# Optimization experiments

Hardware: AMD Instinct MI355X
Metric: run time of the kernel (lower is better)

The kernel has to match this reference:

```python
import jax, jax.numpy as jnp
import numpy as np

N, V, C_IN, C_OUT = 8, 2048, 32, 64
ORDER, SUPPORT_LEN = 2, 3
BN_EPS = 1e-5


def _make_adj(key):
    a = jax.random.uniform(key, (N, V, V), dtype=jnp.float32)
    # row-normalize like a diffusion transition matrix
    return a / jnp.sum(a, axis=-1, keepdims=True)


def setup_inputs() -> dict:
    key = jax.random.key(0)
    ks = jax.random.split(key, 6)
    x = jax.random.normal(ks[0], (N, V, C_IN), dtype=jnp.float32)
    A0 = _make_adj(ks[1])
    A1 = _make_adj(ks[2])
    A2 = _make_adj(ks[3])
    c_in_total = (ORDER * SUPPORT_LEN + 1) * C_IN  # 224
    W = jax.random.normal(ks[4], (C_OUT, c_in_total), dtype=jnp.float32) / np.sqrt(c_in_total)
    b = jnp.zeros((C_OUT,), dtype=jnp.float32)
    gamma = jnp.ones((C_OUT,), dtype=jnp.float32)
    beta = jnp.zeros((C_OUT,), dtype=jnp.float32)
    return {"x": x, "A0": A0, "A1": A1, "A2": A2, "W": W, "b": b,
            "gamma": gamma, "beta": beta}


def reference(x, A0, A1, A2, W, b, gamma, beta):
    # nconv: einsum('nvl,nvw->nwl')
    nconv = lambda h, a: jnp.einsum('nvl,nvw->nwl', h, a)
    out = [x]
    for a in (A0, A1, A2):
        x1 = nconv(x, a)
        out.append(x1)
        for _ in range(2, ORDER + 1):
            x2 = nconv(x1, a)
            out.append(x2)
            x1 = x2
    h = jnp.concatenate(out, axis=-1)            # [N, V, 7*C_IN]
    # 1x1 Conv1d over channel axis == pointwise matmul + bias
    h = jnp.einsum('nvc,oc->nvo', h, W) + b      # [N, V, C_OUT]
    # BatchNorm1d (training-mode batch stats over batch and node dims)
    mean = jnp.mean(h, axis=(0, 1))
    var = jnp.var(h, axis=(0, 1))
    h = (h - mean) * jax.lax.rsqrt(var + BN_EPS) * gamma + beta
    # dropout p=0.0 -> identity
    return h
```

## Files before the change

kernel.cpp:

```cpp
#include <hip/hip_runtime.h>
#include <hip/hip_bf16.h>


#define V    2048
#define NB   8
#define CIN  32
#define COUT 64
#define CTOT 224

typedef __attribute__((ext_vector_type(8))) short bf16x8;
typedef __attribute__((ext_vector_type(16))) float f32x16;

static __device__ __forceinline__ short f2bf(float f) {
  __hip_bfloat16 h = __float2bfloat16(f);
  return *reinterpret_cast<short*>(&h);
}

static __device__ __forceinline__ void gll16(const float* g, float* l) {
  __builtin_amdgcn_global_load_lds(
      (const __attribute__((address_space(1))) void*)g,
      (__attribute__((address_space(3))) void*)l, 16, 0, 0);
}

__global__ __launch_bounds__(256) void nconv_mfma_kernel(
    const float* __restrict__ Adj, const float* __restrict__ Xin,
    float* __restrict__ Xout) {
  __shared__ float S[4][4][2][16][32];

  const int bid  = blockIdx.x;
  const int n    = bid >> 6;
  const int ws   = (bid & 63) * 32;
  const int t    = threadIdx.x;
  const int q    = t >> 6;
  const int lane = t & 63;
  const int g    = lane >> 5;
  const int mn   = lane & 31;

  const float* Abase = Adj + (size_t)n * V * V + (size_t)q * 512 * V + ws;
  const float* Xbase = Xin + (size_t)n * V * CIN + q * 512 * CIN;
  const float* Asrc = Abase + (size_t)(lane >> 3) * V + (lane & 7) * 4;
  const float* Xsrc = Xbase + lane * 4;

  auto stage = [&](int c) {
    const int r = c & 3;
    const float* a = Asrc + (size_t)c * 16 * V;
    const float* x = Xsrc + c * 16 * CIN;
    gll16(a,         &S[q][r][0][0][0]);
    gll16(a + 8 * V, &S[q][r][0][8][0]);
    gll16(x,         &S[q][r][1][0][0]);
    gll16(x + 256,   &S[q][r][1][8][0]);
  };

  f32x16 acc;
#pragma unroll
  for (int r = 0; r < 16; ++r) acc[r] = 0.f;

  auto compute = [&](int r) {
    float a8[8], x8[8];
#pragma unroll
    for (int j = 0; j < 8; ++j) {
      a8[j] = S[q][r][0][8 * g + j][mn];
      x8[j] = S[q][r][1][8 * g + j][mn];
    }
    bf16x8 aop, bop;
#pragma unroll
    for (int j = 0; j < 8; ++j) {
      aop[j] = f2bf(x8[j]);
      bop[j] = f2bf(a8[j]);
    }
    acc = __builtin_amdgcn_mfma_f32_32x32x16_bf16(aop, bop, acc, 0, 0, 0);
  };

  stage(0);
  stage(1);
  stage(2);
#pragma unroll 1
  for (int kk = 0; kk < 29; ++kk) {
    stage(kk + 3);
    asm volatile("s_waitcnt vmcnt(12)" ::: "memory");
    __builtin_amdgcn_sched_barrier(0);
    compute(kk & 3);
  }
  asm volatile("s_waitcnt vmcnt(8)" ::: "memory");
  __builtin_amdgcn_sched_barrier(0);
  compute(29 & 3);
  asm volatile("s_waitcnt vmcnt(4)" ::: "memory");
  __builtin_amdgcn_sched_barrier(0);
  compute(30 & 3);
  asm volatile("s_waitcnt vmcnt(0)" ::: "memory");
  __builtin_amdgcn_sched_barrier(0);
  compute(31 & 3);

  __syncthreads();
  float(*Lred)[32][33] = reinterpret_cast<float(*)[32][33]>(&S[0][0][0][0][0]);
#pragma unroll
  for (int r = 0; r < 16; ++r) {
    Lred[q][(r & 3) + 8 * (r >> 2) + 4 * g][mn] = acc[r];
  }
  __syncthreads();
  const int w  = t >> 3;
  const int l4 = t & 7;
  float4 o;
  float* op = &o.x;
#pragma unroll
  for (int i = 0; i < 4; ++i) {
    op[i] = Lred[0][l4 * 4 + i][w] + Lred[1][l4 * 4 + i][w] +
            Lred[2][l4 * 4 + i][w] + Lred[3][l4 * 4 + i][w];
  }
  *(float4*)(Xout + ((size_t)n * V + ws + w) * CIN + l4 * 4) = o;
}

__global__ __launch_bounds__(256) void conv_bn_stats_kernel(
    const float* __restrict__ W, const float* __restrict__ bias,
    const float* __restrict__ p0, const float* __restrict__ p1,
    const float* __restrict__ p2, const float* __restrict__ p3,
    const float* __restrict__ p4, const float* __restrict__ p5,
    const float* __restrict__ p6, float* __restrict__ hout,
    float* __restrict__ stats) {
  __shared__ float Wl[COUT * CTOT];
  __shared__ float Fl[64 * CTOT];
  const int t = threadIdx.x;
  const int R0 = blockIdx.x * 64;

#pragma unroll
  for (int s = 0; s < 14; ++s) {
    int fl = t + s * 256;
    int o = fl / 56, c4 = fl % 56;
    float4 wv = *(const float4*)(W + o * CTOT + c4 * 4);
    int c = c4 * 4;
    int csw = c ^ (((o >> 2) & 7) << 2);
    *(float4*)&Wl[o * CTOT + csw] = wv;
  }
  const float* parts[7] = {p0, p1, p2, p3, p4, p5, p6};
#pragma unroll
  for (int p = 0; p < 7; ++p) {
    const float* __restrict__ src = parts[p] + (size_t)R0 * CIN;
#pragma unroll
    for (int s = 0; s < 2; ++s) {
      int fl = t + s * 256;
      int r = fl >> 3, c4 = fl & 7;
      float4 v = *(const float4*)(src + r * CIN + c4 * 4);
      int c = p * 32 + c4 * 4;
      int csw = c ^ (((r >> 2) & 7) << 2);
      *(float4*)&Fl[r * CTOT + csw] = v;
    }
  }
  __syncthreads();

  const int rg = t & 15, og = t >> 4;
  const int r0 = rg * 4, o0 = og * 4;
  float acc[4][4];
#pragma unroll
  for (int i = 0; i < 4; ++i)
#pragma unroll
    for (int j = 0; j < 4; ++j) acc[i][j] = bias[o0 + j];

  const int fsw = (rg & 7) << 2;
  const int wsw = (og & 7) << 2;
  for (int cc = 0; cc < CTOT; cc += 4) {
    float4 f[4], w[4];
#pragma unroll
    for (int i = 0; i < 4; ++i)
      f[i] = *(const float4*)&Fl[(r0 + i) * CTOT + (cc ^ fsw)];
#pragma unroll
    for (int j = 0; j < 4; ++j)
      w[j] = *(const float4*)&Wl[(o0 + j) * CTOT + (cc ^ wsw)];
#pragma unroll
    for (int i = 0; i < 4; ++i)
#pragma unroll
      for (int j = 0; j < 4; ++j)
        acc[i][j] += f[i].x * w[j].x + f[i].y * w[j].y + f[i].z * w[j].z +
                     f[i].w * w[j].w;
  }

#pragma unroll
  for (int i = 0; i < 4; ++i) {
    *(float4*)(hout + (size_t)(R0 + r0 + i) * COUT + o0) =
        make_float4(acc[i][0], acc[i][1], acc[i][2], acc[i][3]);
  }

  __syncthreads();
  float* red = Fl;
#pragma unroll
  for (int j = 0; j < 4; ++j) {
    float s = acc[0][j] + acc[1][j] + acc[2][j] + acc[3][j];
    float qq = acc[0][j] * acc[0][j] + acc[1][j] * acc[1][j] +
               acc[2][j] * acc[2][j] + acc[3][j] * acc[3][j];
    red[(o0 + j) * 16 + rg] = s;
    red[1024 + (o0 + j) * 16 + rg] = qq;
  }
  __syncthreads();
  if (t < 128) {
    int o = t & 63, which = t >> 6;
    const float* b = red + which * 1024 + o * 16;
    float v = 0.f;
#pragma unroll
    for (int k = 0; k < 16; ++k) v += b[k];
    atomicAdd(stats + which * COUT + o, v);
  }
}

__global__ __launch_bounds__(256) void bn_apply_kernel(
    float* __restrict__ hout, const float* __restrict__ stats,
    const float* __restrict__ gamma, const float* __restrict__ beta) {
  const int i4 = blockIdx.x * 256 + threadIdx.x;
  const int oi = i4 & 15;
  float4 h = ((const float4*)hout)[i4];
  const float4 s = ((const float4*)stats)[oi];
  const float4 q = ((const float4*)(stats + COUT))[oi];
  const float4 g = ((const float4*)gamma)[oi];
  const float4 bb = ((const float4*)beta)[oi];
  const float inv = 1.f / 16384.f;
  float m, vv, rs;
  m = s.x * inv; vv = q.x * inv - m * m; rs = rsqrtf(vv + 1e-5f);
  h.x = (h.x - m) * rs * g.x + bb.x;
  m = s.y * inv; vv = q.y * inv - m * m; rs = rsqrtf(vv + 1e-5f);
  h.y = (h.y - m) * rs * g.y + bb.y;
  m = s.z * inv; vv = q.z * inv - m * m; rs = rsqrtf(vv + 1e-5f);
  h.z = (h.z - m) * rs * g.z + bb.z;
  m = s.w * inv; vv = q.w * inv - m * m; rs = rsqrtf(vv + 1e-5f);
  h.w = (h.w - m) * rs * g.w + bb.w;
  ((float4*)hout)[i4] = h;
}

extern "C" void kernel_launch(void* const* d_in, const int* in_sizes, int n_in,
                              void* d_out, int out_size, void* d_ws,
                              size_t ws_size, hipStream_t stream) {
  const float* x     = (const float*)d_in[0];
  const float* A0    = (const float*)d_in[1];
  const float* A1    = (const float*)d_in[2];
  const float* A2    = (const float*)d_in[3];
  const float* W     = (const float*)d_in[4];
  const float* b     = (const float*)d_in[5];
  const float* gamma = (const float*)d_in[6];
  const float* beta  = (const float*)d_in[7];
  float* out = (float*)d_out;

  char* ws = (char*)d_ws;
  float* stats = (float*)ws;
  const size_t BUF = (size_t)NB * V * CIN;
  float* x1_0 = (float*)(ws + 4096);
  float* x2_0 = x1_0 + BUF;
  float* x1_1 = x2_0 + BUF;
  float* x2_1 = x1_1 + BUF;
  float* x1_2 = x2_1 + BUF;
  float* x2_2 = x1_2 + BUF;

  hipMemsetAsync(stats, 0, 2 * COUT * sizeof(float), stream);

  dim3 g(512), blk(256);
  nconv_mfma_kernel<<<g, blk, 0, stream>>>(A0, x, x1_0);
  nconv_mfma_kernel<<<g, blk, 0, stream>>>(A0, x1_0, x2_0);
  nconv_mfma_kernel<<<g, blk, 0, stream>>>(A1, x, x1_1);
  nconv_mfma_kernel<<<g, blk, 0, stream>>>(A1, x1_1, x2_1);
  nconv_mfma_kernel<<<g, blk, 0, stream>>>(A2, x, x1_2);
  nconv_mfma_kernel<<<g, blk, 0, stream>>>(A2, x1_2, x2_2);

  conv_bn_stats_kernel<<<dim3(256), blk, 0, stream>>>(
      W, b, x, x1_0, x2_0, x1_1, x2_1, x1_2, x2_2, out, stats);
  bn_apply_kernel<<<dim3(1024), blk, 0, stream>>>(out, stats, gamma, beta);
}
```

Baseline: 204.8 us.

## Split nconv K-reduction across 8 waves with separate A/X staging buffers

The nconv kernel moves from 4 to 8 waves per block, so each wave handles a 256-row K slice instead of 512 and runs 16 MFMA steps instead of 32. The staging buffers are split so A gets a triple buffer and X a double buffer, with new vmcnt wait values. The cross-wave reduction now sums 8 partials, with each thread writing a float2. The aim is more memory parallelism for streaming the adjacency matrix, at the cost of a larger reduction and a shorter pipeline per wave.

```diff
diff --git a/kernel.cpp b/kernel.cpp
--- a/kernel.cpp
+++ b/kernel.cpp
@@ -22,45 +22,48 @@
       (__attribute__((address_space(3))) void*)l, 16, 0, 0);
 }
 
-__global__ __launch_bounds__(256) void nconv_mfma_kernel(
+__global__ __launch_bounds__(512, 4) void nconv_mfma_kernel(
     const float* __restrict__ Adj, const float* __restrict__ Xin,
     float* __restrict__ Xout) {
-  __shared__ float S[4][4][2][16][32];
+  __shared__ float SA[8][3][16][32];
+  __shared__ float SX[8][2][16][32];
 
   const int bid  = blockIdx.x;
   const int n    = bid >> 6;
   const int ws   = (bid & 63) * 32;
   const int t    = threadIdx.x;
-  const int q    = t >> 6;
+  const int wq   = t >> 6;
   const int lane = t & 63;
   const int g    = lane >> 5;
   const int mn   = lane & 31;
 
-  const float* Abase = Adj + (size_t)n * V * V + (size_t)q * 512 * V + ws;
-  const float* Xbase = Xin + (size_t)n * V * CIN + q * 512 * CIN;
-  const float* Asrc = Abase + (size_t)(lane >> 3) * V + (lane & 7) * 4;
-  const float* Xsrc = Xbase + lane * 4;
-
-  auto stage = [&](int c) {
-    const int r = c & 3;
-    const float* a = Asrc + (size_t)c * 16 * V;
-    const float* x = Xsrc + c * 16 * CIN;
-    gll16(a,         &S[q][r][0][0][0]);
-    gll16(a + 8 * V, &S[q][r][0][8][0]);
-    gll16(x,         &S[q][r][1][0][0]);
-    gll16(x + 256,   &S[q][r][1][8][0]);
+  const float* __restrict__ Asrc = Adj + (size_t)n * V * V +
+                                   (size_t)(wq * 256) * V + ws +
+                                   (size_t)(lane >> 3) * V + (lane & 7) * 4;
+  const float* __restrict__ Xsrc =
+      Xin + (size_t)n * V * CIN + wq * 256 * CIN + lane * 4;
+
+  auto stage_a = [&](int slot, int c) {
+    const float* a = Asrc + (size_t)c * (16 * V);
+    gll16(a, &SA[wq][slot][0][0]);
+    gll16(a + 8 * V, &SA[wq][slot][8][0]);
   };
+  auto stage_x = [&](int slot, int c) {
+    const float* x = Xsrc + c * (16 * CIN);
+    gll16(x, &SX[wq][slot][0][0]);
+    gll16(x + 256, &SX[wq][slot][8][0]);
+  };
 
   f32x16 acc;
 #pragma unroll
   for (int r = 0; r < 16; ++r) acc[r] = 0.f;
 
-  auto compute = [&](int r) {
+  auto compute = [&](int sa, int sx) {
     float a8[8], x8[8];
 #pragma unroll
     for (int j = 0; j < 8; ++j) {
-      a8[j] = S[q][r][0][8 * g + j][mn];
-      x8[j] = S[q][r][1][8 * g + j][mn];
+      a8[j] = SA[wq][sa][8 * g + j][mn];
+      x8[j] = SX[wq][sx][8 * g + j][mn];
     }
     bf16x8 aop, bop;
 #pragma unroll
@@ -71,43 +74,55 @@
     acc = __builtin_amdgcn_mfma_f32_32x32x16_bf16(aop, bop, acc, 0, 0, 0);
   };
 
-  stage(0);
-  stage(1);
-  stage(2);
+#define WAITV(N)                                          \
+  do {                                                    \
+    asm volatile("s_waitcnt vmcnt(" #N ")" ::: "memory"); \
+    __builtin_amdgcn_sched_barrier(0);                    \
+  } while (0)
+
+  stage_a(0, 0);
+  stage_x(0, 0);
+  stage_a(1, 1);
+
+  int ca = 0, cx = 0;
 #pragma unroll 1
-  for (int kk = 0; kk < 29; ++kk) {
-    stage(kk + 3);
-    asm volatile("s_waitcnt vmcnt(12)" ::: "memory");
-    __builtin_amdgcn_sched_barrier(0);
-    compute(kk & 3);
-  }
-  asm volatile("s_waitcnt vmcnt(8)" ::: "memory");
-  __builtin_amdgcn_sched_barrier(0);
-  compute(29 & 3);
-  asm volatile("s_waitcnt vmcnt(4)" ::: "memory");
-  __builtin_amdgcn_sched_barrier(0);
-  compute(30 & 3);
-  asm volatile("s_waitcnt vmcnt(0)" ::: "memory");
-  __builtin_amdgcn_sched_barrier(0);
-  compute(31 & 3);
-
-  __syncthreads();
-  float(*Lred)[32][33] = reinterpret_cast<float(*)[32][33]>(&S[0][0][0][0][0]);
+  for (int i = 0; i < 14; ++i) {
+    stage_x(cx ^ 1, i + 1);
+    const int as = (ca == 0) ? 2 : ca - 1;
+    stage_a(as, i + 2);
+    WAITV(6);
+    compute(ca, cx);
+    ca = (ca == 2) ? 0 : ca + 1;
+    cx ^= 1;
+  }
+  stage_x(cx ^ 1, 15);
+  WAITV(4);
+  compute(ca, cx);
+  ca = (ca == 2) ? 0 : ca + 1;
+  cx ^= 1;
+  WAITV(0);
+  compute(ca, cx);
+
+#undef WAITV
+
+  __syncthreads();
+  float(*Lred)[32][33] = reinterpret_cast<float(*)[32][33]>(&SA[0][0][0][0]);
 #pragma unroll
   for (int r = 0; r < 16; ++r) {
-    Lred[q][(r & 3) + 8 * (r >> 2) + 4 * g][mn] = acc[r];
-  }
-  __syncthreads();
-  const int w  = t >> 3;
-  const int l4 = t & 7;
-  float4 o;
-  float* op = &o.x;
-#pragma unroll
-  for (int i = 0; i < 4; ++i) {
-    op[i] = Lred[0][l4 * 4 + i][w] + Lred[1][l4 * 4 + i][w] +
-            Lred[2][l4 * 4 + i][w] + Lred[3][l4 * 4 + i][w];
-  }
-  *(float4*)(Xout + ((size_t)n * V + ws + w) * CIN + l4 * 4) = o;
+    Lred[wq][(r & 3) + 8 * (r >> 2) + 4 * g][mn] = acc[r];
+  }
+  __syncthreads();
+  const int w  = t >> 4;
+  const int l0 = (t & 15) * 2;
+  float2 o;
+  o.x = 0.f;
+  o.y = 0.f;
+#pragma unroll
+  for (int k = 0; k < 8; ++k) {
+    o.x += Lred[k][l0][w];
+    o.y += Lred[k][l0 + 1][w];
+  }
+  *(float2*)(Xout + ((size_t)n * V + ws + w) * CIN + l0) = o;
 }
 
 __global__ __launch_bounds__(256) void conv_bn_stats_kernel(
@@ -248,7 +263,7 @@
 
   hipMemsetAsync(stats, 0, 2 * COUT * sizeof(float), stream);
 
-  dim3 g(512), blk(256);
+  dim3 g(512), blk(512);
   nconv_mfma_kernel<<<g, blk, 0, stream>>>(A0, x, x1_0);
   nconv_mfma_kernel<<<g, blk, 0, stream>>>(A0, x1_0, x2_0);
   nconv_mfma_kernel<<<g, blk, 0, stream>>>(A1, x, x1_1);
@@ -256,7 +271,8 @@
   nconv_mfma_kernel<<<g, blk, 0, stream>>>(A2, x, x1_2);
   nconv_mfma_kernel<<<g, blk, 0, stream>>>(A2, x1_2, x2_2);
 
-  conv_bn_stats_kernel<<<dim3(256), blk, 0, stream>>>(
+  conv_bn_stats_kernel<<<dim3(256), dim3(256), 0, stream>>>(
       W, b, x, x1_0, x2_0, x1_1, x2_1, x1_2, x2_2, out, stats);
-  bn_apply_kernel<<<dim3(1024), blk, 0, stream>>>(out, stats, gamma, beta);
-}
+  bn_apply_kernel<<<dim3(1024), dim3(256), 0, stream>>>(out, stats, gamma,
+                                                        beta);
+}
```

New measurement: 212.2 us. +3.6%, slower.
